# Performance work log

Measured on AMD Instinct MI355X. Metric: run time of the kernel, lower is better.

The kernel has to match this reference:

```python
import jax, jax.numpy as jnp
import numpy as np

N, D = 16384, 128
T = 0.07  # temperature


def setup_inputs() -> dict:
    key = jax.random.key(0)
    x = jax.random.normal(key, (N, D), dtype=jnp.float32)
    # uniformity loss assumes unit-norm embeddings (else exp(||x||^2 / t) overflows)
    x = x / jnp.linalg.norm(x, axis=-1, keepdims=True)
    return {"x": x}


def reference(x):
    # x.matmul(x.T).div(t).exp().sum(-1).log().mean()
    sims = jnp.matmul(x, x.T) / T            # [N, N]
    return jnp.mean(jnp.log(jnp.sum(jnp.exp(sims), axis=-1)))
```

## Files before the change

### kernel.cpp

```cpp
#include <hip/hip_runtime.h>
#include <hip/hip_bf16.h>

#define NN 16384
#define DD 128
#define BM 128
#define BCOLS 4096
#define TCOLS 64
#define TILES 64
#define NBLOCKS 512
#define SQRT_SCALE 4.5398159622f

typedef __attribute__((ext_vector_type(8))) short bf16x8;
typedef __attribute__((ext_vector_type(4))) float f32x4;

__global__ void convert_swz(const float* __restrict__ x, ushort* __restrict__ xb) {
    int t = blockIdx.x * blockDim.x + threadIdx.x;
    int r = t >> 4;
    int c = t & 15;
    const float4* src = (const float4*)(x + (size_t)r * DD + c * 8);
    float4 f0 = src[0];
    float4 f1 = src[1];
    float vals[8] = {f0.x, f0.y, f0.z, f0.w, f1.x, f1.y, f1.z, f1.w};
    bf16x8 v;
#pragma unroll
    for (int i = 0; i < 8; ++i) {
        __hip_bfloat16 h = __float2bfloat16(vals[i] * SQRT_SCALE);
        v[i] = (short)__builtin_bit_cast(unsigned short, h);
    }
    int cs = c ^ (r & 15);
    *(bf16x8*)(xb + (size_t)r * DD + cs * 8) = v;
}

__global__ __launch_bounds__(512, 4) void gemm_exp_stream(const ushort* __restrict__ xb,
                                                          float* __restrict__ rowsumP) {
    __shared__ __align__(16) ushort lB[2][TCOLS * DD];

    const int tid  = threadIdx.x;
    const int lane = tid & 63;
    const int wid  = tid >> 6;
    const int frow = lane & 15;
    const int kq   = lane >> 4;

    const int bid    = blockIdx.x;
    const int cq     = (bid & 7) >> 1;
    const int rstrip = ((bid >> 3) << 1) | (bid & 1);
    const int rw = wid >> 2;
    const int cw = wid & 3;
    const int R0 = rstrip * BM;
    const int C0 = cq * BCOLS;

    auto stage = [&](int buf, int t) {
        const char* g = (const char*)(xb + (size_t)(C0 + t * TCOLS) * DD);
#pragma unroll
        for (int i = 0; i < 2; ++i) {
            int off = (wid * 2 + i) * 1024;
            __builtin_amdgcn_global_load_lds(
                (const __attribute__((address_space(1))) unsigned int*)(g + off + lane * 16),
                (__attribute__((address_space(3))) unsigned int*)((char*)&lB[buf][0] + off),
                16, 0, 0);
        }
    };

    stage(0, 0);

    bf16x8 af[4][4];
#pragma unroll
    for (int m = 0; m < 4; ++m)
#pragma unroll
        for (int kk = 0; kk < 4; ++kk) {
            int ra = R0 + rw * 64 + m * 16 + frow;
            int slot = (kk * 4 + kq) ^ frow;
            af[m][kk] = *(const bf16x8*)(xb + (size_t)ra * DD + slot * 8);
        }

    const int nbase = (cw * 16 + frow) * 256 + ((kq ^ (frow & 3)) << 4);
    int kkoff[4];
#pragma unroll
    for (int kk = 0; kk < 4; ++kk)
        kkoff[kk] = (kk ^ (frow >> 2)) << 6;

    const f32x4 zacc = {0.f, 0.f, 0.f, 0.f};
    float rs[4][4] = {};

    for (int t = 0; t < TILES; ++t) {
        const int cur = t & 1;
        if (t < TILES - 1) {
            stage(cur ^ 1, t + 1);
            asm volatile("s_waitcnt vmcnt(2)" ::: "memory");
        } else {
            asm volatile("s_waitcnt vmcnt(0)" ::: "memory");
        }
        __builtin_amdgcn_s_barrier();

        const char* Bb = (const char*)&lB[cur][0];
        f32x4 acc[4];
#pragma unroll
        for (int kk = 0; kk < 4; ++kk) {
            bf16x8 bfr = *(const bf16x8*)(Bb + nbase + kkoff[kk]);
            __builtin_amdgcn_s_setprio(1);
            if (kk == 0) {
#pragma unroll
                for (int m = 0; m < 4; ++m)
                    acc[m] = __builtin_amdgcn_mfma_f32_16x16x32_bf16(
                        af[m][0], bfr, zacc, 0, 0, 0);
            } else {
#pragma unroll
                for (int m = 0; m < 4; ++m)
                    acc[m] = __builtin_amdgcn_mfma_f32_16x16x32_bf16(
                        af[m][kk], bfr, acc[m], 0, 0, 0);
            }
            __builtin_amdgcn_s_setprio(0);
        }
        __builtin_amdgcn_s_barrier();

#pragma unroll
        for (int m = 0; m < 4; ++m)
#pragma unroll
            for (int j = 0; j < 4; ++j)
                rs[m][j] += __builtin_amdgcn_exp2f(acc[m][j]);
    }

#pragma unroll
    for (int m = 0; m < 4; ++m)
#pragma unroll
        for (int j = 0; j < 4; ++j) {
            float s = rs[m][j];
            s += __shfl_xor(s, 1);
            s += __shfl_xor(s, 2);
            s += __shfl_xor(s, 4);
            s += __shfl_xor(s, 8);
            rs[m][j] = s;
        }

    if (frow == 0) {
        const int p = cq * 4 + cw;
        float* dst = rowsumP + (size_t)p * NN + R0 + rw * 64 + kq * 4;
#pragma unroll
        for (int m = 0; m < 4; ++m) {
            float4 v = {rs[m][0], rs[m][1], rs[m][2], rs[m][3]};
            *(float4*)(dst + m * 16) = v;
        }
    }
}

__global__ void finalize_part(const float* __restrict__ rowsumP,
                              float* __restrict__ partial) {
    const int tid = threadIdx.x;
    const int r = blockIdx.x * 256 + tid;
    float rsum = 0.f;
#pragma unroll
    for (int p = 0; p < 16; ++p)
        rsum += rowsumP[p * NN + r];
    float s = __builtin_amdgcn_logf(rsum) * 0.69314718056f;
#pragma unroll
    for (int o = 1; o < 64; o <<= 1)
        s += __shfl_xor(s, o);
    __shared__ float wsum[4];
    if ((tid & 63) == 0) wsum[tid >> 6] = s;
    __syncthreads();
    if (tid == 0)
        partial[blockIdx.x] = wsum[0] + wsum[1] + wsum[2] + wsum[3];
}

__global__ void finalize_sum(const float* __restrict__ partial, float* __restrict__ out) {
    float s = partial[threadIdx.x];
#pragma unroll
    for (int o = 1; o < 64; o <<= 1)
        s += __shfl_xor(s, o);
    if (threadIdx.x == 0)
        out[0] = s * (1.0f / NN);
}

extern "C" void kernel_launch(void* const* d_in, const int* in_sizes, int n_in,
                              void* d_out, int out_size, void* d_ws, size_t ws_size,
                              hipStream_t stream) {
    const float* x = (const float*)d_in[0];
    float* out = (float*)d_out;

    ushort* xb     = (ushort*)d_ws;
    float* rowsumP = (float*)((char*)d_ws + (size_t)NN * DD * 2);
    float* partial = rowsumP + 16 * NN;

    convert_swz<<<(NN * 16) / 256, 256, 0, stream>>>(x, xb);
    gemm_exp_stream<<<NBLOCKS, 512, 0, stream>>>(xb, rowsumP);
    finalize_part<<<64, 256, 0, stream>>>(rowsumP, partial);
    finalize_sum<<<1, 64, 0, stream>>>(partial, out);
}
```

Before: 81.22 us.

## Give each wave private LDS buffers and drop block-wide barriers

Each wave now stages only its own 16-column slice of the B tile into a private double-buffered LDS region. The loads are prefetched two tiles ahead and gated by per-wave vmcnt waits, so both block-wide s_barrier calls per tile go away. The aim is to remove barrier stalls and let waves drift and overlap the exp work with loads. The cost is that waves sharing a column slice now load it twice, and LDS per block doubles to 64KB, which may cut how many blocks fit on a CU.

```diff
diff --git a/kernel.cpp b/kernel.cpp
--- a/kernel.cpp
+++ b/kernel.cpp
@@ -33,7 +33,7 @@
 
 __global__ __launch_bounds__(512, 4) void gemm_exp_stream(const ushort* __restrict__ xb,
                                                           float* __restrict__ rowsumP) {
-    __shared__ __align__(16) ushort lB[2][TCOLS * DD];
+    __shared__ __align__(16) char lds[8][2][4096];
 
     const int tid  = threadIdx.x;
     const int lane = tid & 63;
@@ -49,19 +49,21 @@
     const int R0 = rstrip * BM;
     const int C0 = cq * BCOLS;
 
+    char* myL = &lds[wid][0][0];
+
     auto stage = [&](int buf, int t) {
-        const char* g = (const char*)(xb + (size_t)(C0 + t * TCOLS) * DD);
+        const char* g = (const char*)(xb + (size_t)(C0 + t * TCOLS + cw * 16) * DD);
 #pragma unroll
-        for (int i = 0; i < 2; ++i) {
-            int off = (wid * 2 + i) * 1024;
+        for (int j = 0; j < 4; ++j) {
             __builtin_amdgcn_global_load_lds(
-                (const __attribute__((address_space(1))) unsigned int*)(g + off + lane * 16),
-                (__attribute__((address_space(3))) unsigned int*)((char*)&lB[buf][0] + off),
+                (const __attribute__((address_space(1))) unsigned int*)(g + j * 1024 + lane * 16),
+                (__attribute__((address_space(3))) unsigned int*)(myL + buf * 4096 + j * 1024),
                 16, 0, 0);
         }
     };
 
     stage(0, 0);
+    stage(1, 1);
 
     bf16x8 af[4][4];
 #pragma unroll
@@ -73,31 +75,25 @@
             af[m][kk] = *(const bf16x8*)(xb + (size_t)ra * DD + slot * 8);
         }
 
-    const int nbase = (cw * 16 + frow) * 256 + ((kq ^ (frow & 3)) << 4);
-    int kkoff[4];
+    int roff[4];
 #pragma unroll
     for (int kk = 0; kk < 4; ++kk)
-        kkoff[kk] = (kk ^ (frow >> 2)) << 6;
+        roff[kk] = frow * 256 + ((((kk << 2) + kq) ^ frow) << 4);
+
+    asm volatile("s_waitcnt vmcnt(0)" ::: "memory");
 
     const f32x4 zacc = {0.f, 0.f, 0.f, 0.f};
     float rs[4][4] = {};
 
     for (int t = 0; t < TILES; ++t) {
         const int cur = t & 1;
-        if (t < TILES - 1) {
-            stage(cur ^ 1, t + 1);
-            asm volatile("s_waitcnt vmcnt(2)" ::: "memory");
-        } else {
-            asm volatile("s_waitcnt vmcnt(0)" ::: "memory");
-        }
-        __builtin_amdgcn_s_barrier();
+        const char* Bb = myL + cur * 4096;
 
-        const char* Bb = (const char*)&lB[cur][0];
         f32x4 acc[4];
+        __builtin_amdgcn_s_setprio(1);
 #pragma unroll
         for (int kk = 0; kk < 4; ++kk) {
-            bf16x8 bfr = *(const bf16x8*)(Bb + nbase + kkoff[kk]);
-            __builtin_amdgcn_s_setprio(1);
+            bf16x8 bfr = *(const bf16x8*)(Bb + roff[kk]);
             if (kk == 0) {
 #pragma unroll
                 for (int m = 0; m < 4; ++m)
@@ -109,15 +105,22 @@
                     acc[m] = __builtin_amdgcn_mfma_f32_16x16x32_bf16(
                         af[m][kk], bfr, acc[m], 0, 0, 0);
             }
-            __builtin_amdgcn_s_setprio(0);
         }
-        __builtin_amdgcn_s_barrier();
+        __builtin_amdgcn_s_setprio(0);
+
+        __builtin_amdgcn_sched_barrier(0);
+        if (t + 2 < TILES) stage(cur, t + 2);
 
 #pragma unroll
         for (int m = 0; m < 4; ++m)
 #pragma unroll
             for (int j = 0; j < 4; ++j)
                 rs[m][j] += __builtin_amdgcn_exp2f(acc[m][j]);
+
+        if (t < TILES - 2)
+            asm volatile("s_waitcnt vmcnt(4)" ::: "memory");
+        else if (t == TILES - 2)
+            asm volatile("s_waitcnt vmcnt(0)" ::: "memory");
     }
 
 #pragma unroll
```

Result: slower. 85.43 us (+5.2%).
